# Kernel optimization log

Hardware: AMD Instinct MI355X
Metric: run time of the kernel (lower is better)

## Reference

```python
import jax, jax.numpy as jnp
import numpy as np

EPS = 1e-7
REG_MAX = 16


def _ciou(b1, b2, eps=EPS):
    # b1, b2: (..., 4) xyxy aligned boxes -> (...,) CIoU
    x11, y11, x21, y21 = b1[..., 0], b1[..., 1], b1[..., 2], b1[..., 3]
    x12, y12, x22, y22 = b2[..., 0], b2[..., 1], b2[..., 2], b2[..., 3]
    inter_w = jnp.clip(jnp.minimum(x21, x22) - jnp.maximum(x11, x12), 0, None)
    inter_h = jnp.clip(jnp.minimum(y21, y22) - jnp.maximum(y11, y12), 0, None)
    inter = inter_w * inter_h
    w1, h1 = x21 - x11, y21 - y11
    w2, h2 = x22 - x12, y22 - y12
    union = w1 * h1 + w2 * h2 - inter + eps
    iou = inter / union
    cw = jnp.maximum(x21, x22) - jnp.minimum(x11, x12)
    ch = jnp.maximum(y21, y22) - jnp.minimum(y11, y12)
    c2 = cw ** 2 + ch ** 2 + eps
    rho2 = ((x11 + x21 - x12 - x22) ** 2 + (y11 + y21 - y12 - y22) ** 2) / 4
    v = (4 / jnp.pi ** 2) * (jnp.arctan(w1 / (h1 + eps)) - jnp.arctan(w2 / (h2 + eps))) ** 2
    alpha = jax.lax.stop_gradient(v / (1 - iou + v + eps))
    return iou - (rho2 / c2 + v * alpha)


def _bbox2dist(anchor_points, bbox, reg_max_minus1):
    # anchor_points (A,2), bbox (B,A,4) -> (B,A,4) ltrb distances
    ap = anchor_points[None]
    lt = ap - bbox[..., :2]
    rb = bbox[..., 2:] - ap
    return jnp.clip(jnp.concatenate([lt, rb], -1), 0.0, reg_max_minus1 - 0.01)


def setup_inputs() -> dict:
    key = jax.random.key(0)
    B, A, RM, NC = 32, 8400, REG_MAX, 80
    ks = jax.random.split(key, 6)
    anchor_points = jax.random.uniform(ks[0], (A, 2), dtype=jnp.float32) * 640.0
    ap = anchor_points[None]
    off_t = jax.random.uniform(ks[1], (B, A, 4), dtype=jnp.float32) * 48.0 + 2.0
    target_bboxes = jnp.concatenate([ap - off_t[..., :2], ap + off_t[..., 2:]], -1)
    off_p = jax.random.uniform(ks[2], (B, A, 4), dtype=jnp.float32) * 48.0 + 2.0
    pred_bboxes = jnp.concatenate([ap - off_p[..., :2], ap + off_p[..., 2:]], -1)
    pred_dist = jax.random.normal(ks[3], (B, A, 4 * RM), dtype=jnp.float32)
    target_scores = jax.random.uniform(ks[4], (B, A, NC), dtype=jnp.float32) * 0.05
    fg_mask = jax.random.bernoulli(ks[5], 0.1, (B, A))
    target_scores_sum = jnp.maximum((target_scores.sum(-1) * fg_mask).sum(), 1.0)
    return dict(pred_dist=pred_dist, pred_bboxes=pred_bboxes,
                anchor_points=anchor_points, target_bboxes=target_bboxes,
                target_scores=target_scores, target_scores_sum=target_scores_sum,
                fg_mask=fg_mask)


def reference(pred_dist, pred_bboxes, anchor_points, target_bboxes,
              target_scores, target_scores_sum, fg_mask):
    B, A = fg_mask.shape
    RM = pred_dist.shape[-1] // 4
    mf = fg_mask.astype(pred_dist.dtype)
    num_fg = mf.sum()
    # CIoU loss, weighted by per-anchor score sum, only on foreground
    weight = target_scores.sum(-1)
    iou = _ciou(pred_bboxes, target_bboxes)
    loss_iou = jnp.where(fg_mask, (1.0 - iou) * weight, 0.0).sum() / target_scores_sum
    # DFL loss
    t = _bbox2dist(anchor_points, target_bboxes, RM - 1)  # (B,A,4), already in [0, RM-1-0.01]
    tl = t.astype(jnp.int32)                               # left bin
    tr = jnp.minimum(tl + 1, RM - 1)                       # right bin
    wl = (tl + 1).astype(t.dtype) - t
    wr = 1.0 - wl
    logp = jax.nn.log_softmax(pred_dist.reshape(B, A, 4, RM), axis=-1)
    ce_l = -jnp.take_along_axis(logp, tl[..., None], axis=-1)[..., 0]
    ce_r = -jnp.take_along_axis(logp, tr[..., None], axis=-1)[..., 0]
    dfl = (ce_l * wl + ce_r * wr).sum(-1)                  # (B,A)
    loss_dfl = jnp.where(fg_mask, dfl, 0.0).sum() / jnp.maximum(num_fg * 4.0, 1.0)
    return loss_iou, loss_dfl
```

## Files before the change

kernel.cpp:

```cpp
#include <hip/hip_runtime.h>
#include <math.h>

#define EPS 1e-7f
#define REG_MAX 16
#define NC 80
#define A_DIM 8400

__global__ __launch_bounds__(256) void bbox_loss_main(
    const float* __restrict__ pred_dist,
    const float* __restrict__ pred_bboxes,
    const float* __restrict__ anchor_points,
    const float* __restrict__ target_bboxes,
    const float* __restrict__ target_scores,
    const int*   __restrict__ fg_mask,
    float* __restrict__ acc)
{
    const int i = blockIdx.x * blockDim.x + threadIdx.x;

    float liou = 0.f, ldfl = 0.f, nfg = 0.f;

    if (fg_mask[i] != 0) {
        nfg = 1.f;
        const int a = i % A_DIM;
        const float ax = anchor_points[2 * a + 0];
        const float ay = anchor_points[2 * a + 1];

        const float4 pb = *(const float4*)(pred_bboxes + (size_t)i * 4);
        const float4 tb = *(const float4*)(target_bboxes + (size_t)i * 4);

        const float4* ts = (const float4*)(target_scores + (size_t)i * NC);
        float w = 0.f;
        #pragma unroll
        for (int k = 0; k < NC / 4; ++k) {
            float4 v = ts[k];
            w += v.x + v.y + v.z + v.w;
        }

        const float x11 = pb.x, y11 = pb.y, x21 = pb.z, y21 = pb.w;
        const float x12 = tb.x, y12 = tb.y, x22 = tb.z, y22 = tb.w;
        const float iw = fmaxf(fminf(x21, x22) - fmaxf(x11, x12), 0.f);
        const float ih = fmaxf(fminf(y21, y22) - fmaxf(y11, y12), 0.f);
        const float inter = iw * ih;
        const float w1 = x21 - x11, h1 = y21 - y11;
        const float w2 = x22 - x12, h2 = y22 - y12;
        const float uni = w1 * h1 + w2 * h2 - inter + EPS;
        const float iou = inter / uni;
        const float cw = fmaxf(x21, x22) - fminf(x11, x12);
        const float ch = fmaxf(y21, y22) - fminf(y11, y12);
        const float c2 = cw * cw + ch * ch + EPS;
        const float dx = x11 + x21 - x12 - x22;
        const float dy = y11 + y21 - y12 - y22;
        const float rho2 = (dx * dx + dy * dy) * 0.25f;
        const float dang = atanf(w1 / (h1 + EPS)) - atanf(w2 / (h2 + EPS));
        const float v = (4.f / (float)(M_PI * M_PI)) * dang * dang;
        const float alpha = v / (1.f - iou + v + EPS);
        const float ciou = iou - (rho2 / c2 + v * alpha);
        liou = (1.f - ciou) * w;

        float t[4];
        t[0] = fminf(fmaxf(ax - tb.x, 0.f), (float)(REG_MAX - 1) - 0.01f);
        t[1] = fminf(fmaxf(ay - tb.y, 0.f), (float)(REG_MAX - 1) - 0.01f);
        t[2] = fminf(fmaxf(tb.z - ax, 0.f), (float)(REG_MAX - 1) - 0.01f);
        t[3] = fminf(fmaxf(tb.w - ay, 0.f), (float)(REG_MAX - 1) - 0.01f);

        const float* pd = pred_dist + (size_t)i * (4 * REG_MAX);
        float dfl = 0.f;
        #pragma unroll
        for (int s = 0; s < 4; ++s) {
            float x[REG_MAX];
            const float4* p4 = (const float4*)(pd + s * REG_MAX);
            #pragma unroll
            for (int k = 0; k < REG_MAX / 4; ++k) {
                float4 vv = p4[k];
                x[4 * k + 0] = vv.x; x[4 * k + 1] = vv.y;
                x[4 * k + 2] = vv.z; x[4 * k + 3] = vv.w;
            }
            float m = x[0];
            #pragma unroll
            for (int k = 1; k < REG_MAX; ++k) m = fmaxf(m, x[k]);
            float se = 0.f;
            #pragma unroll
            for (int k = 0; k < REG_MAX; ++k) se += __expf(x[k] - m);
            const float lse = m + __logf(se);
            const int tl = (int)t[s];
            const int tr = min(tl + 1, REG_MAX - 1);
            const float wl = (float)(tl + 1) - t[s];
            const float wr = 1.f - wl;
            dfl += (lse - x[tl]) * wl + (lse - x[tr]) * wr;
        }
        ldfl = dfl;
    }

    #pragma unroll
    for (int off = 32; off > 0; off >>= 1) {
        liou += __shfl_down(liou, off);
        ldfl += __shfl_down(ldfl, off);
        nfg  += __shfl_down(nfg, off);
    }
    __shared__ float s0[4], s1[4], s2[4];
    const int wave = threadIdx.x >> 6;
    const int lane = threadIdx.x & 63;
    if (lane == 0) { s0[wave] = liou; s1[wave] = ldfl; s2[wave] = nfg; }
    __syncthreads();
    if (threadIdx.x == 0) {
        float a0 = 0.f, a1 = 0.f, a2 = 0.f;
        #pragma unroll
        for (int k = 0; k < 4; ++k) { a0 += s0[k]; a1 += s1[k]; a2 += s2[k]; }
        atomicAdd(&acc[0], a0);
        atomicAdd(&acc[1], a1);
        atomicAdd(&acc[2], a2);
    }
}

__global__ void bbox_loss_finalize(const float* __restrict__ acc,
                                   const float* __restrict__ tss,
                                   float* __restrict__ out)
{
    out[0] = acc[0] / tss[0];
    out[1] = acc[1] / fmaxf(acc[2] * 4.f, 1.f);
}

extern "C" void kernel_launch(void* const* d_in, const int* in_sizes, int n_in,
                              void* d_out, int out_size, void* d_ws, size_t ws_size,
                              hipStream_t stream) {
    const float* pred_dist     = (const float*)d_in[0];
    const float* pred_bboxes   = (const float*)d_in[1];
    const float* anchor_points = (const float*)d_in[2];
    const float* target_bboxes = (const float*)d_in[3];
    const float* target_scores = (const float*)d_in[4];
    const float* tss           = (const float*)d_in[5];
    const int*   fg_mask       = (const int*)d_in[6];
    float* out = (float*)d_out;
    float* acc = (float*)d_ws;

    const int total = in_sizes[6];
    const int block = 256;
    const int grid = (total + block - 1) / block;

    hipMemsetAsync(acc, 0, 3 * sizeof(float), stream);
    bbox_loss_main<<<grid, block, 0, stream>>>(pred_dist, pred_bboxes, anchor_points,
                                               target_bboxes, target_scores, fg_mask, acc);
    bbox_loss_finalize<<<1, 1, 0, stream>>>(acc, tss, out);
}
```

Measured before the change: 201.1 us.

## Compact foreground indices before the loss kernel to avoid divergent sparse waves

Adds a stream-compaction kernel that uses wave ballots and one atomic per wave to write the indices of foreground anchors into workspace. The main loss kernel then maps threads onto the compacted list, so waves run fully occupied instead of each carrying only about a tenth of its lanes doing work. Blocks with no foreground work also skip their global atomics. The cost is an extra launch, one more pass over the mask and an index indirection, and the index order across waves is nondeterministic.

```diff
diff --git a/kernel.cpp b/kernel.cpp
--- a/kernel.cpp
+++ b/kernel.cpp
@@ -5,6 +5,22 @@
 #define REG_MAX 16
 #define NC 80
 #define A_DIM 8400
+#define TOTAL (32 * 8400)
+
+__global__ __launch_bounds__(256) void fg_compact(
+    const int* __restrict__ fg_mask, int* __restrict__ idx_out, int* __restrict__ count)
+{
+    const int i = blockIdx.x * blockDim.x + threadIdx.x;
+    const bool fg = fg_mask[i] != 0;
+    const unsigned long long ball = __ballot(fg);
+    const int lane = threadIdx.x & 63;
+    const int pre = __popcll(ball & ((1ull << lane) - 1ull));
+    const int tot = __popcll(ball);
+    int base = 0;
+    if (lane == 0 && tot > 0) base = atomicAdd(count, tot);
+    base = __shfl(base, 0);
+    if (fg) idx_out[base + pre] = i;
+}
 
 __global__ __launch_bounds__(256) void bbox_loss_main(
     const float* __restrict__ pred_dist,
@@ -12,14 +28,17 @@
     const float* __restrict__ anchor_points,
     const float* __restrict__ target_bboxes,
     const float* __restrict__ target_scores,
-    const int*   __restrict__ fg_mask,
+    const int* __restrict__ idx,
+    const int* __restrict__ count,
     float* __restrict__ acc)
 {
-    const int i = blockIdx.x * blockDim.x + threadIdx.x;
+    const int j = blockIdx.x * blockDim.x + threadIdx.x;
+    const int n = *count;
 
     float liou = 0.f, ldfl = 0.f, nfg = 0.f;
 
-    if (fg_mask[i] != 0) {
+    if (j < n) {
+        const int i = idx[j];
         nfg = 1.f;
         const int a = i % A_DIM;
         const float ax = anchor_points[2 * a + 0];
@@ -106,9 +125,11 @@
         float a0 = 0.f, a1 = 0.f, a2 = 0.f;
         #pragma unroll
         for (int k = 0; k < 4; ++k) { a0 += s0[k]; a1 += s1[k]; a2 += s2[k]; }
-        atomicAdd(&acc[0], a0);
-        atomicAdd(&acc[1], a1);
-        atomicAdd(&acc[2], a2);
+        if (a2 != 0.f) {
+            atomicAdd(&acc[0], a0);
+            atomicAdd(&acc[1], a1);
+            atomicAdd(&acc[2], a2);
+        }
     }
 }
 
@@ -131,14 +152,18 @@
     const float* tss           = (const float*)d_in[5];
     const int*   fg_mask       = (const int*)d_in[6];
     float* out = (float*)d_out;
-    float* acc = (float*)d_ws;
+
+    float* acc   = (float*)d_ws;
+    int*   count = (int*)((char*)d_ws + 16);
+    int*   idx   = (int*)((char*)d_ws + 64);
 
     const int total = in_sizes[6];
     const int block = 256;
     const int grid = (total + block - 1) / block;
 
-    hipMemsetAsync(acc, 0, 3 * sizeof(float), stream);
+    hipMemsetAsync(d_ws, 0, 32, stream);
+    fg_compact<<<grid, block, 0, stream>>>(fg_mask, idx, count);
     bbox_loss_main<<<grid, block, 0, stream>>>(pred_dist, pred_bboxes, anchor_points,
-                                               target_bboxes, target_scores, fg_mask, acc);
+                                               target_bboxes, target_scores, idx, count, acc);
     bbox_loss_finalize<<<1, 1, 0, stream>>>(acc, tss, out);
 }
```

Result: slower. 216.8 us (+7.8%).

## Compact foreground anchors and process each with a 16-lane group

Applied to the files above, without the earlier changes.

Each block ballot-compacts the foreground anchor indices into shared memory. Sixteen-thread groups then cooperatively process one foreground anchor each: score sum, log-softmax over the DFL bins, and CIoU on one lane. This replaces the per-thread serial path, which was divergent with ~10% occupancy of useful lanes. Global atomics and the memset are replaced by per-block partial sums and a parallel finalize reduction. The risk is extra syncthreads, shuffles, and the CIoU work serialised onto one lane per group.

```diff
diff --git a/kernel.cpp b/kernel.cpp
--- a/kernel.cpp
+++ b/kernel.cpp
@@ -3,121 +3,169 @@
 
 #define EPS 1e-7f
 #define REG_MAX 16
-#define NC 80
 #define A_DIM 8400
 
-__global__ __launch_bounds__(256) void bbox_loss_main(
+
+__global__ __launch_bounds__(256) void bbox_loss_fused(
     const float* __restrict__ pred_dist,
     const float* __restrict__ pred_bboxes,
     const float* __restrict__ anchor_points,
     const float* __restrict__ target_bboxes,
     const float* __restrict__ target_scores,
     const int*   __restrict__ fg_mask,
-    float* __restrict__ acc)
+    float* __restrict__ p_liou,
+    float* __restrict__ p_dfl,
+    float* __restrict__ p_nfg,
+    int total)
 {
-    const int i = blockIdx.x * blockDim.x + threadIdx.x;
+    __shared__ int s_idx[256];
+    __shared__ int s_wtot[4];
+    __shared__ int s_woff[4];
+    __shared__ int s_cnt;
 
-    float liou = 0.f, ldfl = 0.f, nfg = 0.f;
+    const int tid  = threadIdx.x;
+    const int i0   = blockIdx.x * 256 + tid;
+    const int wave = tid >> 6;
+    const int lane = tid & 63;
 
-    if (fg_mask[i] != 0) {
-        nfg = 1.f;
+    const bool fg = (i0 < total) && (fg_mask[i0] != 0);
+    const unsigned long long ball = __ballot(fg);
+    const int pre = __popcll(ball & ((1ull << lane) - 1ull));
+    if (lane == 0) s_wtot[wave] = __popcll(ball);
+    __syncthreads();
+    if (tid == 0) {
+        int off = 0;
+        #pragma unroll
+        for (int k = 0; k < 4; ++k) { s_woff[k] = off; off += s_wtot[k]; }
+        s_cnt = off;
+    }
+    __syncthreads();
+    if (fg) s_idx[s_woff[wave] + pre] = i0;
+    __syncthreads();
+    const int cnt = s_cnt;
+
+    float liou = 0.f, ldfl = 0.f;
+
+    const int g  = tid >> 4;
+    const int gl = tid & 15;
+    const int q  = gl >> 2;
+    const int ql = gl & 3;
+
+    for (int j = g; j < cnt; j += 16) {
+        const int i = s_idx[j];
         const int a = i % A_DIM;
-        const float ax = anchor_points[2 * a + 0];
+
+        const float4* ts4 = (const float4*)(target_scores + (size_t)i * 80);
+        float4 v = ts4[gl];
+        float w = v.x + v.y + v.z + v.w;
+        if (gl < 4) { float4 u = ts4[16 + gl]; w += u.x + u.y + u.z + u.w; }
+        #pragma unroll
+        for (int off = 8; off >= 1; off >>= 1) w += __shfl_xor(w, off);
+
+        const float4 tb = *(const float4*)(target_bboxes + (size_t)i * 4);
+        const float ax = anchor_points[2 * a];
         const float ay = anchor_points[2 * a + 1];
 
-        const float4 pb = *(const float4*)(pred_bboxes + (size_t)i * 4);
-        const float4 tb = *(const float4*)(target_bboxes + (size_t)i * 4);
+        float tq = (q == 0) ? (ax - tb.x) : (q == 1) ? (ay - tb.y)
+                 : (q == 2) ? (tb.z - ax) : (tb.w - ay);
+        tq = fminf(fmaxf(tq, 0.f), (float)(REG_MAX - 1) - 0.01f);
 
-        const float4* ts = (const float4*)(target_scores + (size_t)i * NC);
-        float w = 0.f;
-        #pragma unroll
-        for (int k = 0; k < NC / 4; ++k) {
-            float4 v = ts[k];
-            w += v.x + v.y + v.z + v.w;
+        const float4 x4 = ((const float4*)(pred_dist + (size_t)i * 64))[q * 4 + ql];
+        float m = fmaxf(fmaxf(x4.x, x4.y), fmaxf(x4.z, x4.w));
+        m = fmaxf(m, __shfl_xor(m, 1));
+        m = fmaxf(m, __shfl_xor(m, 2));
+        float se = __expf(x4.x - m) + __expf(x4.y - m)
+                 + __expf(x4.z - m) + __expf(x4.w - m);
+        se += __shfl_xor(se, 1);
+        se += __shfl_xor(se, 2);
+        const float lse = m + __logf(se);
+
+        const int   tl = (int)tq;
+        const int   tr = min(tl + 1, REG_MAX - 1);
+        const float wl = (float)(tl + 1) - tq;
+        const float wr = 1.f - wl;
+        const int base = ql * 4;
+        float s = 0.f;
+        int r = tl - base;
+        if (r >= 0 && r < 4) s += wl * (r == 0 ? x4.x : r == 1 ? x4.y : r == 2 ? x4.z : x4.w);
+        r = tr - base;
+        if (r >= 0 && r < 4) s += wr * (r == 0 ? x4.x : r == 1 ? x4.y : r == 2 ? x4.z : x4.w);
+        s += __shfl_xor(s, 1);
+        s += __shfl_xor(s, 2);
+        if (ql == 0) ldfl += lse - s;
+
+        if (gl == 0) {
+            const float4 pb = *(const float4*)(pred_bboxes + (size_t)i * 4);
+            const float x11 = pb.x, y11 = pb.y, x21 = pb.z, y21 = pb.w;
+            const float x12 = tb.x, y12 = tb.y, x22 = tb.z, y22 = tb.w;
+            const float iw = fmaxf(fminf(x21, x22) - fmaxf(x11, x12), 0.f);
+            const float ih = fmaxf(fminf(y21, y22) - fmaxf(y11, y12), 0.f);
+            const float inter = iw * ih;
+            const float w1 = x21 - x11, h1 = y21 - y11;
+            const float w2 = x22 - x12, h2 = y22 - y12;
+            const float uni = w1 * h1 + w2 * h2 - inter + EPS;
+            const float iou = inter / uni;
+            const float cw = fmaxf(x21, x22) - fminf(x11, x12);
+            const float ch = fmaxf(y21, y22) - fminf(y11, y12);
+            const float c2 = cw * cw + ch * ch + EPS;
+            const float dx = x11 + x21 - x12 - x22;
+            const float dy = y11 + y21 - y12 - y22;
+            const float rho2 = (dx * dx + dy * dy) * 0.25f;
+            const float dang = atanf(w1 / (h1 + EPS)) - atanf(w2 / (h2 + EPS));
+            const float vv = (4.f / (float)(M_PI * M_PI)) * dang * dang;
+            const float alpha = vv / (1.f - iou + vv + EPS);
+            const float ciou = iou - (rho2 / c2 + vv * alpha);
+            liou += (1.f - ciou) * w;
         }
-
-        const float x11 = pb.x, y11 = pb.y, x21 = pb.z, y21 = pb.w;
-        const float x12 = tb.x, y12 = tb.y, x22 = tb.z, y22 = tb.w;
-        const float iw = fmaxf(fminf(x21, x22) - fmaxf(x11, x12), 0.f);
-        const float ih = fmaxf(fminf(y21, y22) - fmaxf(y11, y12), 0.f);
-        const float inter = iw * ih;
-        const float w1 = x21 - x11, h1 = y21 - y11;
-        const float w2 = x22 - x12, h2 = y22 - y12;
-        const float uni = w1 * h1 + w2 * h2 - inter + EPS;
-        const float iou = inter / uni;
-        const float cw = fmaxf(x21, x22) - fminf(x11, x12);
-        const float ch = fmaxf(y21, y22) - fminf(y11, y12);
-        const float c2 = cw * cw + ch * ch + EPS;
-        const float dx = x11 + x21 - x12 - x22;
-        const float dy = y11 + y21 - y12 - y22;
-        const float rho2 = (dx * dx + dy * dy) * 0.25f;
-        const float dang = atanf(w1 / (h1 + EPS)) - atanf(w2 / (h2 + EPS));
-        const float v = (4.f / (float)(M_PI * M_PI)) * dang * dang;
-        const float alpha = v / (1.f - iou + v + EPS);
-        const float ciou = iou - (rho2 / c2 + v * alpha);
-        liou = (1.f - ciou) * w;
-
-        float t[4];
-        t[0] = fminf(fmaxf(ax - tb.x, 0.f), (float)(REG_MAX - 1) - 0.01f);
-        t[1] = fminf(fmaxf(ay - tb.y, 0.f), (float)(REG_MAX - 1) - 0.01f);
-        t[2] = fminf(fmaxf(tb.z - ax, 0.f), (float)(REG_MAX - 1) - 0.01f);
-        t[3] = fminf(fmaxf(tb.w - ay, 0.f), (float)(REG_MAX - 1) - 0.01f);
-
-        const float* pd = pred_dist + (size_t)i * (4 * REG_MAX);
-        float dfl = 0.f;
-        #pragma unroll
-        for (int s = 0; s < 4; ++s) {
-            float x[REG_MAX];
-            const float4* p4 = (const float4*)(pd + s * REG_MAX);
-            #pragma unroll
-            for (int k = 0; k < REG_MAX / 4; ++k) {
-                float4 vv = p4[k];
-                x[4 * k + 0] = vv.x; x[4 * k + 1] = vv.y;
-                x[4 * k + 2] = vv.z; x[4 * k + 3] = vv.w;
-            }
-            float m = x[0];
-            #pragma unroll
-            for (int k = 1; k < REG_MAX; ++k) m = fmaxf(m, x[k]);
-            float se = 0.f;
-            #pragma unroll
-            for (int k = 0; k < REG_MAX; ++k) se += __expf(x[k] - m);
-            const float lse = m + __logf(se);
-            const int tl = (int)t[s];
-            const int tr = min(tl + 1, REG_MAX - 1);
-            const float wl = (float)(tl + 1) - t[s];
-            const float wr = 1.f - wl;
-            dfl += (lse - x[tl]) * wl + (lse - x[tr]) * wr;
-        }
-        ldfl = dfl;
     }
 
     #pragma unroll
-    for (int off = 32; off > 0; off >>= 1) {
+    for (int off = 32; off >= 1; off >>= 1) {
         liou += __shfl_down(liou, off);
         ldfl += __shfl_down(ldfl, off);
-        nfg  += __shfl_down(nfg, off);
     }
-    __shared__ float s0[4], s1[4], s2[4];
-    const int wave = threadIdx.x >> 6;
-    const int lane = threadIdx.x & 63;
-    if (lane == 0) { s0[wave] = liou; s1[wave] = ldfl; s2[wave] = nfg; }
+    __shared__ float r0[4], r1[4];
+    if (lane == 0) { r0[wave] = liou; r1[wave] = ldfl; }
     __syncthreads();
-    if (threadIdx.x == 0) {
-        float a0 = 0.f, a1 = 0.f, a2 = 0.f;
-        #pragma unroll
-        for (int k = 0; k < 4; ++k) { a0 += s0[k]; a1 += s1[k]; a2 += s2[k]; }
-        atomicAdd(&acc[0], a0);
-        atomicAdd(&acc[1], a1);
-        atomicAdd(&acc[2], a2);
+    if (tid == 0) {
+        p_liou[blockIdx.x] = r0[0] + r0[1] + r0[2] + r0[3];
+        p_dfl[blockIdx.x]  = r1[0] + r1[1] + r1[2] + r1[3];
+        p_nfg[blockIdx.x]  = (float)cnt;
     }
 }
 
-__global__ void bbox_loss_finalize(const float* __restrict__ acc,
-                                   const float* __restrict__ tss,
-                                   float* __restrict__ out)
+__global__ __launch_bounds__(256) void bbox_loss_finalize(
+    const float* __restrict__ p_liou,
+    const float* __restrict__ p_dfl,
+    const float* __restrict__ p_nfg,
+    int nb,
+    const float* __restrict__ tss,
+    float* __restrict__ out)
 {
-    out[0] = acc[0] / tss[0];
-    out[1] = acc[1] / fmaxf(acc[2] * 4.f, 1.f);
+    const int tid = threadIdx.x;
+    float a = 0.f, b = 0.f, c = 0.f;
+    for (int k = tid; k < nb; k += 256) {
+        a += p_liou[k];
+        b += p_dfl[k];
+        c += p_nfg[k];
+    }
+    #pragma unroll
+    for (int off = 32; off >= 1; off >>= 1) {
+        a += __shfl_down(a, off);
+        b += __shfl_down(b, off);
+        c += __shfl_down(c, off);
+    }
+    __shared__ float r0[4], r1[4], r2[4];
+    const int wave = tid >> 6, lane = tid & 63;
+    if (lane == 0) { r0[wave] = a; r1[wave] = b; r2[wave] = c; }
+    __syncthreads();
+    if (tid == 0) {
+        const float A = r0[0] + r0[1] + r0[2] + r0[3];
+        const float Bs = r1[0] + r1[1] + r1[2] + r1[3];
+        const float C = r2[0] + r2[1] + r2[2] + r2[3];
+        out[0] = A / tss[0];
+        out[1] = Bs / fmaxf(C * 4.f, 1.f);
+    }
 }
 
 extern "C" void kernel_launch(void* const* d_in, const int* in_sizes, int n_in,
@@ -131,14 +179,16 @@
     const float* tss           = (const float*)d_in[5];
     const int*   fg_mask       = (const int*)d_in[6];
     float* out = (float*)d_out;
-    float* acc = (float*)d_ws;
+
+    float* p_liou = (float*)d_ws;
+    float* p_dfl  = p_liou + 2048;
+    float* p_nfg  = p_liou + 4096;
 
     const int total = in_sizes[6];
-    const int block = 256;
-    const int grid = (total + block - 1) / block;
+    const int nb = (total + 255) / 256;
 
-    hipMemsetAsync(acc, 0, 3 * sizeof(float), stream);
-    bbox_loss_main<<<grid, block, 0, stream>>>(pred_dist, pred_bboxes, anchor_points,
-                                               target_bboxes, target_scores, fg_mask, acc);
-    bbox_loss_finalize<<<1, 1, 0, stream>>>(acc, tss, out);
+    bbox_loss_fused<<<nb, 256, 0, stream>>>(pred_dist, pred_bboxes, anchor_points,
+                                            target_bboxes, target_scores, fg_mask,
+                                            p_liou, p_dfl, p_nfg, total);
+    bbox_loss_finalize<<<1, 256, 0, stream>>>(p_liou, p_dfl, p_nfg, nb, tss, out);
 }
```

After: 167.6 us. 1.2x faster.
